# Optimization experiments

Measured on AMD Instinct MI355X. Metric: run time of the kernel, lower is better.

## Reference

```python
import jax, jax.numpy as jnp
import numpy as np

B, J, I, N = 128, 32, 1152, 16
SPARSE_TOPK = [0.3, 0.3]  # parsed from '0.3;0.3'


def squash(s, axis=-1):
    # v = (|s|^2 / (1 + |s|^2)) * s / |s|
    sq = jnp.sum(s * s, axis=axis, keepdims=True)
    return (sq / (1.0 + sq)) * s / jnp.sqrt(sq)


def setup_inputs() -> dict:
    key = jax.random.key(0)
    u_hat = jax.random.normal(key, (B, J, I, N), dtype=jnp.float32)
    # bias_routing=True -> Parameter(zeros(j,n)).fill_(0.1)
    bias = jnp.full((J, N), 0.1, dtype=jnp.float32)
    return {"u_hat": u_hat, "bias": bias, "iters": 3}


def reference(u_hat, bias, iters):
    b = u_hat.shape[0]
    b_vec = jnp.zeros((b, J, I), dtype=u_hat.dtype)
    stats = []
    v_vec = None
    for index in range(iters):
        # routing coefficients: softmax over output capsules j
        c_vec = jax.nn.softmax(b_vec, axis=1)  # [b,j,i]
        # entropy over dim=1, mean over remaining dims (calc_entropy(...).mean())
        c_safe = jnp.where(c_vec > 0, c_vec, 1.0)
        ent = -jnp.sum(c_vec * jnp.log(c_safe), axis=1)  # [b,i]
        stats.append(jnp.mean(ent))
        # s_vec = (c_vec[b,j,1,i] @ u_hat[b,j,i,n]).squeeze()
        s_vec = jnp.einsum('bji,bjin->bjn', c_vec, u_hat)
        # bias + reset of all-zero rows
        s_vec_bias = s_vec + bias
        reset_mask = (jnp.sum(s_vec, axis=2) == 0)[..., None]  # [b,j,1]
        s_vec_bias = jnp.where(reset_mask, 0.0, s_vec_bias)
        v_vec = squash(s_vec_bias)  # [b,j,n]
        if index < iters - 1:
            # agreement update: u_hat[b,j,i,1,n] @ v_vec[b,j,1,n,1] -> [b,j,i]
            b_vec = b_vec + jnp.einsum('bjin,bjn->bji', u_hat, v_vec)
            # sparsify_edges_topk: mask bottom-k along j per (b,i) column
            mask_count = int(SPARSE_TOPK[index] * J)
            if mask_count > 0:
                # kth smallest along j == max of bottom-k (-inf sorts first, as in torch.topk smallest)
                kth = jnp.sort(b_vec, axis=1)[:, mask_count - 1:mask_count, :]  # [b,1,i]
                b_vec = jnp.where(b_vec <= kth, -jnp.inf, b_vec)
    return v_vec, jnp.stack(stats)
```

## Files before the change

kernel.cpp:

```cpp
#include <hip/hip_runtime.h>
#include <math.h>


#define NB 128
#define NJ 32
#define NI 1152
#define NN 16
#define TI 32
#define NTILES (NI / TI)
#define COLS_TOTAL (NB * NI)

__global__ __launch_bounds__(256) void k_reduce_s0(const float* __restrict__ u,
                                                   float* __restrict__ s0) {
  int bj = blockIdx.x;
  const float4* u4 = (const float4*)u + (size_t)bj * (NI * NN / 4);
  int t = threadIdx.x;
  float4 acc = make_float4(0.f, 0.f, 0.f, 0.f);
#pragma unroll
  for (int k = 0; k < 18; ++k) {
    float4 x = u4[t + 256 * k];
    acc.x += x.x; acc.y += x.y; acc.z += x.z; acc.w += x.w;
  }
#pragma unroll
  for (int m = 4; m <= 32; m <<= 1) {
    acc.x += __shfl_xor(acc.x, m);
    acc.y += __shfl_xor(acc.y, m);
    acc.z += __shfl_xor(acc.z, m);
    acc.w += __shfl_xor(acc.w, m);
  }
  __shared__ float4 parts[4][4];
  int lane = t & 63, w = t >> 6;
  if (lane < 4) parts[w][lane] = acc;
  __syncthreads();
  if (t < 4) {
    float4 p0 = parts[0][t], p1 = parts[1][t], p2 = parts[2][t], p3 = parts[3][t];
    float4 r;
    r.x = (p0.x + p1.x + p2.x + p3.x) * (1.0f / 32.0f);
    r.y = (p0.y + p1.y + p2.y + p3.y) * (1.0f / 32.0f);
    r.z = (p0.z + p1.z + p2.z + p3.z) * (1.0f / 32.0f);
    r.w = (p0.w + p1.w + p2.w + p3.w) * (1.0f / 32.0f);
    ((float4*)(s0 + (size_t)bj * NN))[t] = r;
  }
}

__global__ __launch_bounds__(256) void k_squash(const float* __restrict__ s,
                                                const float* __restrict__ bias,
                                                float* __restrict__ vout,
                                                const float* __restrict__ ent,
                                                int write_stats) {
  int gid = blockIdx.x * 256 + threadIdx.x;
  int vec = gid >> 4, n = gid & 15;
  int j = vec & 31;
  float sv = s[gid];
  float ssum = sv;
#pragma unroll
  for (int m = 1; m < 16; m <<= 1) ssum += __shfl_xor(ssum, m);
  float sb = sv + bias[j * NN + n];
  if (ssum == 0.0f) sb = 0.0f;
  float sq = sb * sb;
#pragma unroll
  for (int m = 1; m < 16; m <<= 1) sq += __shfl_xor(sq, m);
  vout[gid] = (sq / (1.0f + sq)) * sb / sqrtf(sq);
  if (write_stats && gid < 3) {
    float val = (gid == 0) ? logf(32.0f) : ent[gid - 1] / (float)COLS_TOTAL;
    vout[NB * NJ * NN + gid] = val;
  }
}

template <int SPARS>
__global__ __launch_bounds__(256, 2) void k_route(const float* __restrict__ u,
                                                  const float* __restrict__ vprev,
                                                  const float* __restrict__ v0,
                                                  float* __restrict__ kth0,
                                                  float* __restrict__ s_out,
                                                  float* __restrict__ ent_accum) {
  __shared__ __align__(16) float U[16384];
  __shared__ __align__(16) float vA[512];
  __shared__ __align__(16) float vB[512];
  __shared__ float bcols[32 * 37];
  __shared__ float ctile[32 * 37];
  __shared__ float entc[32];

  int t = threadIdx.x;
  int bid = blockIdx.x;
  int b = bid / NTILES;
  int tile = bid - b * NTILES;
  int i0 = tile * TI;
  const float4* ub4 = (const float4*)(u + (size_t)b * (NJ * NI * NN) + (size_t)i0 * NN);

#pragma unroll
  for (int m = 0; m < 16; ++m) {
    int g = m * 256 + t;
    int j = g >> 7;
    int L = ((j >> 3) << 10) + ((g & 3) << 8) + ((j & 7) << 5) + ((g >> 2) & 31);
    float4 x = ub4[g + j * 4480];
    *(float4*)&U[4 * L] = x;
  }
  {
    const float4* vprev4 = (const float4*)(vprev + (size_t)b * (NJ * NN));
    if (t < 128) ((float4*)vA)[t] = vprev4[t];
    if (SPARS == 0) {
      const float4* v04 = (const float4*)(v0 + (size_t)b * (NJ * NN));
      if (t >= 128) ((float4*)vB)[t - 128] = v04[t - 128];
    }
  }
  __syncthreads();

  {
    int col = t & 31;
    int jg = t >> 5;
    float kthcol = 0.f;
    if (SPARS == 0) kthcol = kth0[b * NI + i0 + col];
#pragma unroll
    for (int q2 = 0; q2 < 4; ++q2) {
      int j = q2 * 8 + jg;
      float accA = 0.f, accB = 0.f;
#pragma unroll
      for (int q = 0; q < 4; ++q) {
        float4 uu = *(const float4*)&U[(q2 << 12) + (q << 10) + 4 * t];
        float4 va = *(const float4*)&vA[j * 16 + q * 4];
        accA = fmaf(uu.x, va.x, accA);
        accA = fmaf(uu.y, va.y, accA);
        accA = fmaf(uu.z, va.z, accA);
        accA = fmaf(uu.w, va.w, accA);
        if (SPARS == 0) {
          float4 vb = *(const float4*)&vB[j * 16 + q * 4];
          accB = fmaf(uu.x, vb.x, accB);
          accB = fmaf(uu.y, vb.y, accB);
          accB = fmaf(uu.z, vb.z, accB);
          accB = fmaf(uu.w, vb.w, accB);
        }
      }
      float bv;
      if (SPARS)
        bv = accA;
      else
        bv = ((accB <= kthcol) ? -INFINITY : accB) + accA;
      bcols[col * 37 + j] = bv;
    }
  }
  __syncthreads();

  {
    int col = t >> 3, sg = t & 7;
    float own0 = bcols[col * 37 + sg * 4 + 0];
    float own1 = bcols[col * 37 + sg * 4 + 1];
    float own2 = bcols[col * 37 + sg * 4 + 2];
    float own3 = bcols[col * 37 + sg * 4 + 3];
    float m;
    if (SPARS) {
      int r0 = 0, r1 = 0, r2 = 0, r3 = 0, e0 = 0, e1 = 0, e2 = 0, e3 = 0;
      m = -INFINITY;
#pragma unroll
      for (int jj = 0; jj < 32; ++jj) {
        float bj = bcols[col * 37 + jj];
        m = fmaxf(m, bj);
        r0 += (bj < own0); e0 += (bj == own0);
        r1 += (bj < own1); e1 += (bj == own1);
        r2 += (bj < own2); e2 += (bj == own2);
        r3 += (bj < own3); e3 += (bj == own3);
      }
      float cand = -INFINITY;
      if (r0 <= 8 && 8 < r0 + e0) cand = fmaxf(cand, own0);
      if (r1 <= 8 && 8 < r1 + e1) cand = fmaxf(cand, own1);
      if (r2 <= 8 && 8 < r2 + e2) cand = fmaxf(cand, own2);
      if (r3 <= 8 && 8 < r3 + e3) cand = fmaxf(cand, own3);
      cand = fmaxf(cand, __shfl_xor(cand, 1));
      cand = fmaxf(cand, __shfl_xor(cand, 2));
      cand = fmaxf(cand, __shfl_xor(cand, 4));
      if (own0 <= cand) own0 = -INFINITY;
      if (own1 <= cand) own1 = -INFINITY;
      if (own2 <= cand) own2 = -INFINITY;
      if (own3 <= cand) own3 = -INFINITY;
      if (sg == 0) kth0[b * NI + i0 + col] = cand;
    } else {
      float lm = fmaxf(fmaxf(own0, own1), fmaxf(own2, own3));
      lm = fmaxf(lm, __shfl_xor(lm, 1));
      lm = fmaxf(lm, __shfl_xor(lm, 2));
      lm = fmaxf(lm, __shfl_xor(lm, 4));
      m = lm;
    }
    float x0 = expf(own0 - m), x1 = expf(own1 - m);
    float x2 = expf(own2 - m), x3 = expf(own3 - m);
    float ps = (x0 + x1) + (x2 + x3);
    ps += __shfl_xor(ps, 1);
    ps += __shfl_xor(ps, 2);
    ps += __shfl_xor(ps, 4);
    float c0 = x0 / ps, c1 = x1 / ps, c2 = x2 / ps, c3 = x3 / ps;
    ctile[col * 37 + sg * 4 + 0] = c0;
    ctile[col * 37 + sg * 4 + 1] = c1;
    ctile[col * 37 + sg * 4 + 2] = c2;
    ctile[col * 37 + sg * 4 + 3] = c3;
    float ent = 0.f;
    if (c0 > 0.f) ent += c0 * logf(c0);
    if (c1 > 0.f) ent += c1 * logf(c1);
    if (c2 > 0.f) ent += c2 * logf(c2);
    if (c3 > 0.f) ent += c3 * logf(c3);
    ent += __shfl_xor(ent, 1);
    ent += __shfl_xor(ent, 2);
    ent += __shfl_xor(ent, 4);
    if (sg == 0) entc[col] = -ent;
  }
  __syncthreads();

  {
    int j = t >> 3, np = t & 7;
    int q = np >> 1, half = np & 1;
    int jg = j & 7, q2 = j >> 3;
    const float* Ub = &U[(q2 << 12) + (q << 10) + (jg << 7) + 2 * half];
    int coff = (np + j) & 31;
    float acc0 = 0.f, acc1 = 0.f;
#pragma unroll
    for (int cc = 0; cc < 32; ++cc) {
      int col = (cc + coff) & 31;
      float c = ctile[col * 37 + j];
      float2 uu = *(const float2*)&Ub[4 * col];
      acc0 = fmaf(c, uu.x, acc0);
      acc1 = fmaf(c, uu.y, acc1);
    }
    int outi = (b * NJ + j) * NN + 2 * np;
    unsafeAtomicAdd(&s_out[outi], acc0);
    unsafeAtomicAdd(&s_out[outi + 1], acc1);
  }
  if (t < 32) {
    float e = entc[t];
    e += __shfl_xor(e, 1);
    e += __shfl_xor(e, 2);
    e += __shfl_xor(e, 4);
    e += __shfl_xor(e, 8);
    e += __shfl_xor(e, 16);
    if (t == 0) unsafeAtomicAdd(ent_accum, e);
  }
}

extern "C" void kernel_launch(void* const* d_in, const int* in_sizes, int n_in,
                              void* d_out, int out_size, void* d_ws, size_t ws_size,
                              hipStream_t stream) {
  (void)in_sizes; (void)n_in; (void)out_size; (void)ws_size;
  const float* u = (const float*)d_in[0];
  const float* bias = (const float*)d_in[1];
  float* ws = (float*)d_ws;
  float* s1 = ws;
  float* s2 = ws + 65536;
  float* ent = ws + 131072;
  float* s0 = ws + 131076;
  float* v0 = ws + 196612;
  float* v1 = ws + 262148;
  float* kth0 = ws + 327684;
  float* dout = (float*)d_out;

  hipMemsetAsync(d_ws, 0, (size_t)(131072 + 4) * sizeof(float), stream);

  k_reduce_s0<<<dim3(NB * NJ), dim3(256), 0, stream>>>(u, s0);
  k_squash<<<dim3(256), dim3(256), 0, stream>>>(s0, bias, v0, (const float*)nullptr, 0);
  k_route<1><<<dim3(NB * NTILES), dim3(256), 0, stream>>>(u, v0, (const float*)nullptr,
                                                          kth0, s1, ent + 0);
  k_squash<<<dim3(256), dim3(256), 0, stream>>>(s1, bias, v1, (const float*)nullptr, 0);
  k_route<0><<<dim3(NB * NTILES), dim3(256), 0, stream>>>(u, v1, v0, kth0, s2, ent + 1);
  k_squash<<<dim3(256), dim3(256), 0, stream>>>(s2, bias, dout, ent, 1);
}
```

Baseline: 580.5 us.

## Keep u_hat tile in registers instead of LDS in routing kernel

The routing kernel now holds each thread's 4 columns × 16 elements of u_hat in registers rather than staging the 64KB tile in shared memory, and computes the agreement dot products directly from those registers. The weighted sum s is reduced with a butterfly shuffle-exchange across the 8 column-group lanes before the atomics. The score and coefficient arrays use a swizzled 33-stride layout to avoid bank conflicts. This removes the large LDS footprint, which allows more blocks per CU. The cost is higher register pressure (64 floats held per thread) and less coalesced global loads, since each thread reads a strided 64B chunk.

After: 573.1 us. No clear change (-1.3%).

```diff
diff --git a/kernel.cpp b/kernel.cpp
--- a/kernel.cpp
+++ b/kernel.cpp
@@ -9,6 +9,10 @@
 #define TI 32
 #define NTILES (NI / TI)
 #define COLS_TOTAL (NB * NI)
+
+__device__ __forceinline__ int bca(int j, int col) {
+  return j * 33 + ((col + 4 * j) & 31);
+}
 
 __global__ __launch_bounds__(256) void k_reduce_s0(const float* __restrict__ u,
                                                    float* __restrict__ s0) {
@@ -49,8 +53,8 @@
                                                 const float* __restrict__ ent,
                                                 int write_stats) {
   int gid = blockIdx.x * 256 + threadIdx.x;
-  int vec = gid >> 4, n = gid & 15;
-  int j = vec & 31;
+  int n = gid & 15;
+  int j = (gid >> 4) & 31;
   float sv = s[gid];
   float ssum = sv;
 #pragma unroll
@@ -68,17 +72,14 @@
 }
 
 template <int SPARS>
-__global__ __launch_bounds__(256, 2) void k_route(const float* __restrict__ u,
-                                                  const float* __restrict__ vprev,
-                                                  const float* __restrict__ v0,
-                                                  float* __restrict__ kth0,
-                                                  float* __restrict__ s_out,
-                                                  float* __restrict__ ent_accum) {
-  __shared__ __align__(16) float U[16384];
-  __shared__ __align__(16) float vA[512];
-  __shared__ __align__(16) float vB[512];
-  __shared__ float bcols[32 * 37];
-  __shared__ float ctile[32 * 37];
+__global__ __launch_bounds__(256) void k_route(const float* __restrict__ u,
+                                               const float* __restrict__ vprev,
+                                               const float* __restrict__ v0,
+                                               float* __restrict__ kth0,
+                                               float* __restrict__ s_out,
+                                               float* __restrict__ ent_accum) {
+  __shared__ float bc[32 * 33];
+  __shared__ float ct[32 * 33];
   __shared__ float entc[32];
 
   int t = threadIdx.x;
@@ -86,74 +87,68 @@
   int b = bid / NTILES;
   int tile = bid - b * NTILES;
   int i0 = tile * TI;
-  const float4* ub4 = (const float4*)(u + (size_t)b * (NJ * NI * NN) + (size_t)i0 * NN);
-
-#pragma unroll
-  for (int m = 0; m < 16; ++m) {
-    int g = m * 256 + t;
-    int j = g >> 7;
-    int L = ((j >> 3) << 10) + ((g & 3) << 8) + ((j & 7) << 5) + ((g >> 2) & 31);
-    float4 x = ub4[g + j * 4480];
-    *(float4*)&U[4 * L] = x;
-  }
-  {
-    const float4* vprev4 = (const float4*)(vprev + (size_t)b * (NJ * NN));
-    if (t < 128) ((float4*)vA)[t] = vprev4[t];
-    if (SPARS == 0) {
-      const float4* v04 = (const float4*)(v0 + (size_t)b * (NJ * NN));
-      if (t >= 128) ((float4*)vB)[t - 128] = v04[t - 128];
-    }
-  }
-  __syncthreads();
-
-  {
-    int col = t & 31;
-    int jg = t >> 5;
-    float kthcol = 0.f;
-    if (SPARS == 0) kthcol = kth0[b * NI + i0 + col];
-#pragma unroll
-    for (int q2 = 0; q2 < 4; ++q2) {
-      int j = q2 * 8 + jg;
-      float accA = 0.f, accB = 0.f;
-#pragma unroll
-      for (int q = 0; q < 4; ++q) {
-        float4 uu = *(const float4*)&U[(q2 << 12) + (q << 10) + 4 * t];
-        float4 va = *(const float4*)&vA[j * 16 + q * 4];
-        accA = fmaf(uu.x, va.x, accA);
-        accA = fmaf(uu.y, va.y, accA);
-        accA = fmaf(uu.z, va.z, accA);
-        accA = fmaf(uu.w, va.w, accA);
-        if (SPARS == 0) {
-          float4 vb = *(const float4*)&vB[j * 16 + q * 4];
-          accB = fmaf(uu.x, vb.x, accB);
-          accB = fmaf(uu.y, vb.y, accB);
-          accB = fmaf(uu.z, vb.z, accB);
-          accB = fmaf(uu.w, vb.w, accB);
-        }
+  int j = t >> 3, cg = t & 7;
+
+  const float4* up = (const float4*)u + ((size_t)(b * NJ + j) * NI + i0 + cg) * 4;
+  float4 Ur[4][4];
+#pragma unroll
+  for (int k = 0; k < 4; ++k)
+#pragma unroll
+    for (int q = 0; q < 4; ++q) Ur[k][q] = up[k * 32 + q];
+
+  float kthc[4];
+  if (SPARS == 0) {
+#pragma unroll
+    for (int k = 0; k < 4; ++k) kthc[k] = kth0[b * NI + i0 + cg + 8 * k];
+  }
+  const float4* vA4 = (const float4*)vprev + (b * NJ + j) * 4;
+  const float4* vB4 = (const float4*)v0 + (b * NJ + j) * 4;
+  float accA[4] = {0.f, 0.f, 0.f, 0.f};
+  float accB[4] = {0.f, 0.f, 0.f, 0.f};
+#pragma unroll
+  for (int q = 0; q < 4; ++q) {
+    float4 vaq = vA4[q];
+    float4 vbq;
+    if (SPARS == 0) vbq = vB4[q];
+#pragma unroll
+    for (int k = 0; k < 4; ++k) {
+      float4 uu = Ur[k][q];
+      accA[k] = fmaf(uu.x, vaq.x, accA[k]);
+      accA[k] = fmaf(uu.y, vaq.y, accA[k]);
+      accA[k] = fmaf(uu.z, vaq.z, accA[k]);
+      accA[k] = fmaf(uu.w, vaq.w, accA[k]);
+      if (SPARS == 0) {
+        accB[k] = fmaf(uu.x, vbq.x, accB[k]);
+        accB[k] = fmaf(uu.y, vbq.y, accB[k]);
+        accB[k] = fmaf(uu.z, vbq.z, accB[k]);
+        accB[k] = fmaf(uu.w, vbq.w, accB[k]);
       }
-      float bv;
-      if (SPARS)
-        bv = accA;
-      else
-        bv = ((accB <= kthcol) ? -INFINITY : accB) + accA;
-      bcols[col * 37 + j] = bv;
-    }
+    }
+  }
+#pragma unroll
+  for (int k = 0; k < 4; ++k) {
+    float bv;
+    if (SPARS)
+      bv = accA[k];
+    else
+      bv = ((accB[k] <= kthc[k]) ? -INFINITY : accB[k]) + accA[k];
+    bc[bca(j, cg + 8 * k)] = bv;
   }
   __syncthreads();
 
   {
     int col = t >> 3, sg = t & 7;
-    float own0 = bcols[col * 37 + sg * 4 + 0];
-    float own1 = bcols[col * 37 + sg * 4 + 1];
-    float own2 = bcols[col * 37 + sg * 4 + 2];
-    float own3 = bcols[col * 37 + sg * 4 + 3];
+    float own0 = bc[bca(sg * 4 + 0, col)];
+    float own1 = bc[bca(sg * 4 + 1, col)];
+    float own2 = bc[bca(sg * 4 + 2, col)];
+    float own3 = bc[bca(sg * 4 + 3, col)];
     float m;
     if (SPARS) {
       int r0 = 0, r1 = 0, r2 = 0, r3 = 0, e0 = 0, e1 = 0, e2 = 0, e3 = 0;
       m = -INFINITY;
 #pragma unroll
       for (int jj = 0; jj < 32; ++jj) {
-        float bj = bcols[col * 37 + jj];
+        float bj = bc[bca(jj, col)];
         m = fmaxf(m, bj);
         r0 += (bj < own0); e0 += (bj == own0);
         r1 += (bj < own1); e1 += (bj == own1);
@@ -187,10 +182,10 @@
     ps += __shfl_xor(ps, 2);
     ps += __shfl_xor(ps, 4);
     float c0 = x0 / ps, c1 = x1 / ps, c2 = x2 / ps, c3 = x3 / ps;
-    ctile[col * 37 + sg * 4 + 0] = c0;
-    ctile[col * 37 + sg * 4 + 1] = c1;
-    ctile[col * 37 + sg * 4 + 2] = c2;
-    ctile[col * 37 + sg * 4 + 3] = c3;
+    ct[bca(sg * 4 + 0, col)] = c0;
+    ct[bca(sg * 4 + 1, col)] = c1;
+    ct[bca(sg * 4 + 2, col)] = c2;
+    ct[bca(sg * 4 + 3, col)] = c3;
     float ent = 0.f;
     if (c0 > 0.f) ent += c0 * logf(c0);
     if (c1 > 0.f) ent += c1 * logf(c1);
@@ -204,23 +199,46 @@
   __syncthreads();
 
   {
-    int j = t >> 3, np = t & 7;
-    int q = np >> 1, half = np & 1;
-    int jg = j & 7, q2 = j >> 3;
-    const float* Ub = &U[(q2 << 12) + (q << 10) + (jg << 7) + 2 * half];
-    int coff = (np + j) & 31;
-    float acc0 = 0.f, acc1 = 0.f;
-#pragma unroll
-    for (int cc = 0; cc < 32; ++cc) {
-      int col = (cc + coff) & 31;
-      float c = ctile[col * 37 + j];
-      float2 uu = *(const float2*)&Ub[4 * col];
-      acc0 = fmaf(c, uu.x, acc0);
-      acc1 = fmaf(c, uu.y, acc1);
-    }
-    int outi = (b * NJ + j) * NN + 2 * np;
-    unsafeAtomicAdd(&s_out[outi], acc0);
-    unsafeAtomicAdd(&s_out[outi + 1], acc1);
+    float part[16];
+#pragma unroll
+    for (int n = 0; n < 16; ++n) part[n] = 0.f;
+#pragma unroll
+    for (int k = 0; k < 4; ++k) {
+      float c = ct[bca(j, cg + 8 * k)];
+#pragma unroll
+      for (int q = 0; q < 4; ++q) {
+        float4 uu = Ur[k][q];
+        part[4 * q + 0] = fmaf(c, uu.x, part[4 * q + 0]);
+        part[4 * q + 1] = fmaf(c, uu.y, part[4 * q + 1]);
+        part[4 * q + 2] = fmaf(c, uu.z, part[4 * q + 2]);
+        part[4 * q + 3] = fmaf(c, uu.w, part[4 * q + 3]);
+      }
+    }
+    float nw[8];
+#pragma unroll
+    for (int i = 0; i < 8; ++i) {
+      float send = (cg & 1) ? part[i] : part[i + 8];
+      float recv = __shfl_xor(send, 1);
+      nw[i] = ((cg & 1) ? part[i + 8] : part[i]) + recv;
+    }
+    float n2[4];
+#pragma unroll
+    for (int i = 0; i < 4; ++i) {
+      float send = (cg & 2) ? nw[i] : nw[i + 4];
+      float recv = __shfl_xor(send, 2);
+      n2[i] = ((cg & 2) ? nw[i + 4] : nw[i]) + recv;
+    }
+    float n3[2];
+#pragma unroll
+    for (int i = 0; i < 2; ++i) {
+      float send = (cg & 4) ? n2[i] : n2[i + 2];
+      float recv = __shfl_xor(send, 4);
+      n3[i] = ((cg & 4) ? n2[i + 2] : n2[i]) + recv;
+    }
+    int base = (cg & 1) * 8 + (cg & 2) * 2 + ((cg & 4) >> 1);
+    int outi = (b * NJ + j) * NN + base;
+    unsafeAtomicAdd(&s_out[outi], n3[0]);
+    unsafeAtomicAdd(&s_out[outi + 1], n3[1]);
   }
   if (t < 32) {
     float e = entc[t];
@@ -253,8 +271,7 @@
 
   k_reduce_s0<<<dim3(NB * NJ), dim3(256), 0, stream>>>(u, s0);
   k_squash<<<dim3(256), dim3(256), 0, stream>>>(s0, bias, v0, (const float*)nullptr, 0);
-  k_route<1><<<dim3(NB * NTILES), dim3(256), 0, stream>>>(u, v0, (const float*)nullptr,
-                                                          kth0, s1, ent + 0);
+  k_route<1><<<dim3(NB * NTILES), dim3(256), 0, stream>>>(u, v0, v0, kth0, s1, ent + 0);
   k_squash<<<dim3(256), dim3(256), 0, stream>>>(s1, bias, v1, (const float*)nullptr, 0);
   k_route<0><<<dim3(NB * NTILES), dim3(256), 0, stream>>>(u, v1, v0, kth0, s2, ent + 1);
   k_squash<<<dim3(256), dim3(256), 0, stream>>>(s2, bias, dout, ent, 1);
```
